# Optimization experiments

Hardware: AMD Instinct MI355X
Metric: run time of the kernel (lower is better)

## Reference

```python
import jax, jax.numpy as jnp
import numpy as np

T, B, D = 2048, 4, 1024

def setup_inputs() -> dict:
    key = jax.random.key(0)
    ks = jax.random.split(key, 4)
    return {
        "query": jax.random.normal(ks[0], (T, B, D), jnp.float32),
        "input_feature": jax.random.normal(ks[1], (T, B, D), jnp.float32),
        "in_proj_weight": jax.random.normal(ks[2], (2 * D, D), jnp.float32) * (D ** -0.5),
        "in_proj_bias": jnp.zeros((2 * D,), jnp.float32),
        "out_proj_weight": jax.random.normal(ks[3], (D, D), jnp.float32) * (D ** -0.5),
        "out_proj_bias": jnp.zeros((D,), jnp.float32),
    }

def reference(query, input_feature, in_proj_weight, in_proj_bias, out_proj_weight, out_proj_bias):
    d = query.shape[-1]
    scaling = d ** -0.5
    # joint KV projection: [T,B,2D], then chunk
    kv = jnp.einsum('tbd,ed->tbe', input_feature, in_proj_weight) + in_proj_bias
    k, v = kv[..., :d], kv[..., d:]
    q = query * scaling
    # attn_weights: [B, T(query), S(key)]
    attn_weights = jnp.einsum('tbd,sbd->bts', q, k)
    attn_weights = jax.nn.softmax(attn_weights.astype(jnp.float32), axis=-1).astype(q.dtype)
    # attn: [B,T,D] -> [T,B,D]
    attn = jnp.einsum('bts,sbd->tbd', attn_weights, v)
    attn = jnp.einsum('tbd,ed->tbe', attn, out_proj_weight) + out_proj_bias
    return attn, attn_weights
```

## Files before the change

kernel.cpp:

```cpp
#include <hip/hip_runtime.h>
#include <hip/hip_bf16.h>
#include <type_traits>

static constexpr int T = 2048;
static constexpr int B = 4;
static constexpr int D = 1024;
static constexpr int E = 2 * D;
static constexpr int M1 = T * B;

typedef __attribute__((ext_vector_type(8))) short short8;
typedef __attribute__((ext_vector_type(4))) float f32x4;

__device__ inline ushort f2bf(float x) {
    __hip_bfloat16 h = __float2bfloat16(x);
    return __builtin_bit_cast(ushort, h);
}

__device__ inline void glds16(const void* g, void* l) {
    __builtin_amdgcn_global_load_lds(
        (const __attribute__((address_space(1))) void*)g,
        (__attribute__((address_space(3))) void*)l, 16, 0, 0);
}

__device__ inline void xcd_swizzle(int nx, int ny, int& bn_i, int& bm_i) {
    int id = blockIdx.y * nx + blockIdx.x;
    const int q = (nx * ny) >> 3;
    id = (id & 7) * q + (id >> 3);
    bm_i = id / nx;
    bn_i = id - bm_i * nx;
}

template <typename OT>
__device__ __forceinline__ void gemm_body(
    const ushort* __restrict__ A, const ushort* __restrict__ Bt,
    OT* __restrict__ C, const float* __restrict__ bias,
    int K, int lda, int ldb, int ldc, float alpha, int bm, int bn)
{
    __shared__ ushort As[128 * 64];
    __shared__ ushort Bs[128 * 64];

    const int tid  = threadIdx.x;
    const int lane = tid & 63;
    const int wave = tid >> 6;
    const int wm = (wave & 1) * 64;
    const int wn = (wave >> 1) * 64;

    f32x4 acc[4][4] = {};

    const int srow  = lane >> 3;
    const int sElem = (((lane & 7) ^ (lane >> 3))) * 8;
    const int rbase = ((lane >> 4) ^ (lane & 7)) * 8;
    const int rxor4 = 4 * 8;

    for (int k0 = 0; k0 < K; k0 += 64) {
        __syncthreads();
#pragma unroll
        for (int j = 0; j < 4; ++j) {
            const int r = wave * 32 + j * 8;
            glds16(Bt + (long long)(bn + r + srow) * ldb + (k0 + sElem),
                   (void*)&Bs[r * 64]);
            glds16(A + (long long)(bm + r + srow) * lda + (k0 + sElem),
                   (void*)&As[r * 64]);
        }
        __syncthreads();

#pragma unroll
        for (int kb = 0; kb < 2; ++kb) {
            const int rElem = rbase ^ (kb ? rxor4 : 0);
            short8 af[4], bf[4];
#pragma unroll
            for (int i = 0; i < 4; ++i) {
                const int m = wm + i * 16 + (lane & 15);
                af[i] = *(const short8*)&As[m * 64 + rElem];
            }
#pragma unroll
            for (int j = 0; j < 4; ++j) {
                const int n = wn + j * 16 + (lane & 15);
                bf[j] = *(const short8*)&Bs[n * 64 + rElem];
            }
#pragma unroll
            for (int i = 0; i < 4; ++i)
#pragma unroll
                for (int j = 0; j < 4; ++j)
                    acc[i][j] = __builtin_amdgcn_mfma_f32_16x16x32_bf16(af[i], bf[j], acc[i][j], 0, 0, 0);
        }
    }

#pragma unroll
    for (int j = 0; j < 4; ++j) {
        const int col = bn + wn + j * 16 + (lane & 15);
        const float bv = bias ? bias[col] : 0.0f;
#pragma unroll
        for (int i = 0; i < 4; ++i) {
            const int row0 = bm + wm + i * 16 + ((lane >> 4) << 2);
#pragma unroll
            for (int r = 0; r < 4; ++r) {
                const float v = acc[i][j][r] * alpha + bv;
                if constexpr (std::is_same<OT, float>::value)
                    C[(long long)(row0 + r) * ldc + col] = v;
                else
                    C[(long long)(row0 + r) * ldc + col] = f2bf(v);
            }
        }
    }
}

__device__ __forceinline__ void cast_blk(const float* __restrict__ s,
                                         ushort* __restrict__ d, int blk) {
    const int i = blk * 256 + threadIdx.x;
    const float4 v = ((const float4*)s)[i];
    ushort4 o;
    o.x = f2bf(v.x); o.y = f2bf(v.y); o.z = f2bf(v.z); o.w = f2bf(v.w);
    ((ushort4*)d)[i] = o;
}

__device__ __forceinline__ void transpose_body(const ushort* __restrict__ kv,
                                               ushort* __restrict__ vt,
                                               int s0, int d0, int b) {
    __shared__ ushort tile[64][65];
    const int t = threadIdx.x;
    const int dl = (t & 15) * 4, sl = t >> 4;
#pragma unroll
    for (int p = 0; p < 4; ++p) {
        const int s = sl + p * 16;
        const ushort4 v = *(const ushort4*)&kv[((long long)(s0 + s) * B + b) * E + D + d0 + dl];
        tile[s][dl + 0] = v.x; tile[s][dl + 1] = v.y;
        tile[s][dl + 2] = v.z; tile[s][dl + 3] = v.w;
    }
    __syncthreads();
    const int dl2 = t >> 4, sl2 = (t & 15) * 4;
#pragma unroll
    for (int p = 0; p < 4; ++p) {
        const int d = dl2 + p * 16;
        ushort4 o;
        o.x = tile[sl2 + 0][d]; o.y = tile[sl2 + 1][d];
        o.z = tile[sl2 + 2][d]; o.w = tile[sl2 + 3][d];
        *(ushort4*)&vt[(long long)b * D * T + (long long)(d0 + d) * T + s0 + sl2] = o;
    }
}

__global__ __launch_bounds__(256) void cast_xw(
    const float* __restrict__ x, ushort* __restrict__ xbf,
    const float* __restrict__ w_in, ushort* __restrict__ wibf)
{
    const int blk = blockIdx.x;
    if (blk < 8192) cast_blk(x, xbf, blk);
    else            cast_blk(w_in, wibf, blk - 8192);
}

__global__ __launch_bounds__(256) void g1_cast(
    const ushort* __restrict__ xbf, const ushort* __restrict__ wibf,
    ushort* __restrict__ kv, const float* __restrict__ b_in,
    const float* __restrict__ query, ushort* __restrict__ qbf,
    const float* __restrict__ w_out, ushort* __restrict__ wobf)
{
    if (blockIdx.y < 64) {
        int bn_i, bm_i;
        xcd_swizzle(16, 64, bn_i, bm_i);
        gemm_body<ushort>(xbf, wibf, kv, b_in, D, D, D, E, 1.0f,
                          bm_i * 128, bn_i * 128);
    } else {
        const int idx = (blockIdx.y - 64) * 16 + blockIdx.x;
        if (idx < 8192) cast_blk(query, qbf, idx);
        else            cast_blk(w_out, wobf, idx - 8192);
    }
}

__global__ __launch_bounds__(256) void qk_trans(
    const ushort* __restrict__ qbf, const ushort* __restrict__ kv,
    float* __restrict__ out_w, ushort* __restrict__ vt)
{
    const int b = blockIdx.z;
    if (blockIdx.y < 16) {
        int bn_i, bm_i;
        xcd_swizzle(16, 16, bn_i, bm_i);
        gemm_body<float>(qbf + (long long)b * D, kv + (long long)b * E,
                         out_w + (long long)b * T * T, nullptr,
                         D, B * D, B * E, T, 0.03125f,
                         bm_i * 128, bn_i * 128);
    } else {
        const int idx = (blockIdx.y - 16) * 16 + blockIdx.x;
        transpose_body(kv, vt, (idx & 31) * 64, (idx >> 5) * 64, b);
    }
}

template <typename OT>
__global__ __launch_bounds__(256) void mfma_gemm_nt(
    const ushort* __restrict__ A, const ushort* __restrict__ Bt,
    OT* __restrict__ C, const float* __restrict__ bias,
    int K, int lda, int ldb, int ldc,
    long long aBatch, long long bBatch, long long cBatch, float alpha)
{
    int bn_i, bm_i;
    xcd_swizzle(gridDim.x, gridDim.y, bn_i, bm_i);
    gemm_body<OT>(A + blockIdx.z * aBatch, Bt + blockIdx.z * bBatch,
                  C + blockIdx.z * cBatch, bias,
                  K, lda, ldb, ldc, alpha, bm_i * 128, bn_i * 128);
}

__global__ __launch_bounds__(256) void softmax_kernel(float* __restrict__ W,
                                                      ushort* __restrict__ Pbf)
{
    const long long row = blockIdx.x;
    float* p = W + row * (long long)T;
    ushort* pb = Pbf + row * (long long)T;
    const int tid = threadIdx.x;

    float4 v0 = ((const float4*)p)[tid];
    float4 v1 = ((const float4*)p)[tid + 256];

    float m = fmaxf(fmaxf(fmaxf(v0.x, v0.y), fmaxf(v0.z, v0.w)),
                    fmaxf(fmaxf(v1.x, v1.y), fmaxf(v1.z, v1.w)));
#pragma unroll
    for (int off = 1; off < 64; off <<= 1) m = fmaxf(m, __shfl_xor(m, off));

    __shared__ float red[4];
    const int wid = tid >> 6, lane = tid & 63;
    if (lane == 0) red[wid] = m;
    __syncthreads();
    m = fmaxf(fmaxf(red[0], red[1]), fmaxf(red[2], red[3]));
    __syncthreads();

    v0.x = expf(v0.x - m); v0.y = expf(v0.y - m);
    v0.z = expf(v0.z - m); v0.w = expf(v0.w - m);
    v1.x = expf(v1.x - m); v1.y = expf(v1.y - m);
    v1.z = expf(v1.z - m); v1.w = expf(v1.w - m);

    float s = v0.x + v0.y + v0.z + v0.w + v1.x + v1.y + v1.z + v1.w;
#pragma unroll
    for (int off = 1; off < 64; off <<= 1) s += __shfl_xor(s, off);
    if (lane == 0) red[wid] = s;
    __syncthreads();
    s = red[0] + red[1] + red[2] + red[3];

    const float inv = 1.0f / s;
    v0.x *= inv; v0.y *= inv; v0.z *= inv; v0.w *= inv;
    v1.x *= inv; v1.y *= inv; v1.z *= inv; v1.w *= inv;

    ((float4*)p)[tid] = v0;
    ((float4*)p)[tid + 256] = v1;

    ushort4 o0, o1;
    o0.x = f2bf(v0.x); o0.y = f2bf(v0.y); o0.z = f2bf(v0.z); o0.w = f2bf(v0.w);
    o1.x = f2bf(v1.x); o1.y = f2bf(v1.y); o1.z = f2bf(v1.z); o1.w = f2bf(v1.w);
    ((ushort4*)pb)[tid] = o0;
    ((ushort4*)pb)[tid + 256] = o1;
}

extern "C" void kernel_launch(void* const* d_in, const int* in_sizes, int n_in,
                              void* d_out, int out_size, void* d_ws, size_t ws_size,
                              hipStream_t stream)
{
    const float* query = (const float*)d_in[0];
    const float* x     = (const float*)d_in[1];
    const float* w_in  = (const float*)d_in[2];
    const float* b_in  = (const float*)d_in[3];
    const float* w_out = (const float*)d_in[4];
    const float* b_out = (const float*)d_in[5];

    float* out_attn = (float*)d_out;
    float* out_w    = out_attn + (long long)T * B * D;

    char* ws = (char*)d_ws;
    ushort* xbf  = (ushort*)(ws);
    ushort* amid = (ushort*)(ws);
    ushort* qbf  = (ushort*)(ws + (16ll << 20));
    ushort* wibf = (ushort*)(ws + (32ll << 20));
    ushort* wobf = (ushort*)(ws + (36ll << 20));
    ushort* kv   = (ushort*)(ws + (38ll << 20));
    ushort* Pbf  = (ushort*)(ws + (38ll << 20));
    ushort* vt   = (ushort*)(ws + (70ll << 20));

    cast_xw<<<dim3(8192 + 2048), 256, 0, stream>>>(x, xbf, w_in, wibf);

    g1_cast<<<dim3(16, 64 + 576), 256, 0, stream>>>(
        xbf, wibf, kv, b_in, query, qbf, w_out, wobf);

    qk_trans<<<dim3(16, 48, 4), 256, 0, stream>>>(qbf, kv, out_w, vt);

    softmax_kernel<<<dim3(B * T), 256, 0, stream>>>(out_w, Pbf);

    mfma_gemm_nt<ushort><<<dim3(D / 128, T / 128, B), 256, 0, stream>>>(
        Pbf, vt, amid, nullptr, T, T, T, B * D,
        (long long)T * T, (long long)D * T, (long long)D, 1.0f);

    mfma_gemm_nt<float><<<dim3(D / 128, M1 / 128, 1), 256, 0, stream>>>(
        amid, wobf, out_attn, b_out, D, D, D, D, 0, 0, 0, 1.0f);
}
```

Baseline: 354.1 us.

## Interleave GEMM tiles with cast/transpose blocks in fused kernels' 1D grid

Both fused kernels move from 2D/3D grids that launched all GEMM blocks first to a 1D grid. In that grid, groups of 8 GEMM tiles alternate with groups of 8 memory-bound cast or transpose blocks. A new tile mapping spreads GEMM tiles across XCDs (g&7 selects a row stripe) in place of the previous xcd_swizzle. The aim is to overlap compute-bound MFMA work with bandwidth-bound work on the same CUs and cut the tail, at some risk to L2 locality of the GEMM tiles.

```diff
diff --git a/kernel.cpp b/kernel.cpp
--- a/kernel.cpp
+++ b/kernel.cpp
@@ -139,6 +139,20 @@
     }
 }
 
+__device__ __forceinline__ bool interleave_decode(int id, int& sub) {
+    if (id < 2048) {
+        const int grp = id >> 3, w = id & 7;
+        sub = (grp >> 1) * 8 + w;
+        return (grp & 1) == 0;
+    }
+    sub = 1024 + (id - 2048);
+    return false;
+}
+
+__device__ __forceinline__ int gemm_tile_of(int g) {
+    return (g & 7) * 128 + (g >> 3);
+}
+
 __global__ __launch_bounds__(256) void cast_xw(
     const float* __restrict__ x, ushort* __restrict__ xbf,
     const float* __restrict__ w_in, ushort* __restrict__ wibf)
@@ -154,15 +168,14 @@
     const float* __restrict__ query, ushort* __restrict__ qbf,
     const float* __restrict__ w_out, ushort* __restrict__ wobf)
 {
-    if (blockIdx.y < 64) {
-        int bn_i, bm_i;
-        xcd_swizzle(16, 64, bn_i, bm_i);
+    int sub;
+    if (interleave_decode(blockIdx.x, sub)) {
+        const int tile = gemm_tile_of(sub);
         gemm_body<ushort>(xbf, wibf, kv, b_in, D, D, D, E, 1.0f,
-                          bm_i * 128, bn_i * 128);
+                          (tile >> 4) * 128, (tile & 15) * 128);
     } else {
-        const int idx = (blockIdx.y - 64) * 16 + blockIdx.x;
-        if (idx < 8192) cast_blk(query, qbf, idx);
-        else            cast_blk(w_out, wobf, idx - 8192);
+        if (sub < 8192) cast_blk(query, qbf, sub);
+        else            cast_blk(w_out, wobf, sub - 8192);
     }
 }
 
@@ -170,16 +183,16 @@
     const ushort* __restrict__ qbf, const ushort* __restrict__ kv,
     float* __restrict__ out_w, ushort* __restrict__ vt)
 {
-    const int b = blockIdx.z;
-    if (blockIdx.y < 16) {
-        int bn_i, bm_i;
-        xcd_swizzle(16, 16, bn_i, bm_i);
+    int sub;
+    if (interleave_decode(blockIdx.x, sub)) {
+        const int tile = gemm_tile_of(sub);
+        const int b = tile >> 8, t = tile & 255;
         gemm_body<float>(qbf + (long long)b * D, kv + (long long)b * E,
                          out_w + (long long)b * T * T, nullptr,
                          D, B * D, B * E, T, 0.03125f,
-                         bm_i * 128, bn_i * 128);
+                         (t >> 4) * 128, (t & 15) * 128);
     } else {
-        const int idx = (blockIdx.y - 16) * 16 + blockIdx.x;
+        const int b = sub >> 9, idx = sub & 511;
         transpose_body(kv, vt, (idx & 31) * 64, (idx >> 5) * 64, b);
     }
 }
@@ -273,10 +286,10 @@
 
     cast_xw<<<dim3(8192 + 2048), 256, 0, stream>>>(x, xbf, w_in, wibf);
 
-    g1_cast<<<dim3(16, 64 + 576), 256, 0, stream>>>(
+    g1_cast<<<dim3(10240), 256, 0, stream>>>(
         xbf, wibf, kv, b_in, query, qbf, w_out, wobf);
 
-    qk_trans<<<dim3(16, 48, 4), 256, 0, stream>>>(qbf, kv, out_w, vt);
+    qk_trans<<<dim3(3072), 256, 0, stream>>>(qbf, kv, out_w, vt);
 
     softmax_kernel<<<dim3(B * T), 256, 0, stream>>>(out_w, Pbf);
 
```

New measurement: 419.8 us. +18.5%, slower.
